# Kernel optimization log

Hardware: AMD Instinct MI355X
Metric: run time of the kernel (lower is better)

## Reference

```python
import jax, jax.numpy as jnp
import numpy as np

B_SZ, SEQ, IN_F, OUT_F, ST_F = 16, 4096, 256, 256, 256
RMIN, RMAX, MAX_PHASE = 0.9, 1.0, 6.283


def setup_inputs() -> dict:
    key = jax.random.key(0)
    ks = jax.random.split(key, 8)
    u1 = jax.random.uniform(ks[0], (ST_F,))
    u2 = jax.random.uniform(ks[1], (ST_F,))
    # same init math as the torch module
    nu_log = jnp.log(-0.5 * jnp.log(u1 * (RMAX + RMIN) * (RMAX - RMIN) + RMIN ** 2))
    theta_log = jnp.log(MAX_PHASE * u2)
    lam_abs = jnp.exp(-jnp.exp(nu_log))
    gamma_log = jnp.log(jnp.sqrt(1.0 - lam_abs ** 2))
    s2in = np.sqrt(2.0 * IN_F)
    B_re = jax.random.normal(ks[2], (ST_F, IN_F)) / s2in
    B_im = jax.random.normal(ks[3], (ST_F, IN_F)) / s2in
    sst = np.sqrt(ST_F)
    C_re = jax.random.normal(ks[4], (OUT_F, ST_F)) / sst
    C_im = jax.random.normal(ks[5], (OUT_F, ST_F)) / sst
    D = jax.random.normal(ks[6], (OUT_F, IN_F)) / np.sqrt(IN_F)
    inp = jax.random.normal(ks[7], (B_SZ, SEQ, IN_F), dtype=jnp.float32)
    return {"input": inp, "nu_log": nu_log, "theta_log": theta_log,
            "gamma_log": gamma_log, "B_re": B_re, "B_im": B_im,
            "C_re": C_re, "C_im": C_im, "D": D}


def _binop(a, b):
    # diagonal linear recurrence combine: (A, Bu)
    return (a[0] * b[0], b[0] * a[1] + b[1])


def reference(input, nu_log, theta_log, gamma_log, B_re, B_im, C_re, C_im, D):
    lam_abs = jnp.exp(-jnp.exp(nu_log))
    lam = (lam_abs * jnp.exp(1j * jnp.exp(theta_log))).astype(jnp.complex64)  # [N]
    gam = jnp.exp(gamma_log)[:, None]                                        # [N,1]
    Bm = (gam * (B_re + 1j * B_im)).astype(jnp.complex64)                    # [N,Hin]
    Cm = (C_re + 1j * C_im).astype(jnp.complex64)                            # [Hout,N]
    # Bu_t = B @ u_t  -> [B,L,N]
    Bu = jnp.einsum('blh,nh->bln', input.astype(jnp.complex64), Bm)
    lam_el = jnp.broadcast_to(lam, Bu.shape)
    # parallel associative scan over time: s_t = lam*s_{t-1} + Bu_t, s_{-1}=0
    _, s = jax.lax.associative_scan(_binop, (lam_el, Bu), axis=1)
    # module records the state BEFORE each update (initial state is zero)
    zero0 = jnp.zeros((input.shape[0], 1, lam.shape[0]), dtype=jnp.complex64)
    inner_states = jnp.concatenate([zero0, s[:, :-1, :]], axis=1)            # [B,L,N]
    output = jnp.einsum('bln,on->blo', inner_states, Cm).real \
             + jnp.einsum('blh,oh->blo', input, D)
    return output, inner_states
```

## Files before the change

kernel.cpp:

```cpp
#include <hip/hip_runtime.h>


typedef float  f32x4 __attribute__((ext_vector_type(4)));
typedef short  s16x8 __attribute__((ext_vector_type(8)));

__device__ __forceinline__ unsigned short f2bf(float x) {
  unsigned int u = __builtin_bit_cast(unsigned int, x);
  u += 0x7FFFu + ((u >> 16) & 1u);
  return (unsigned short)(u >> 16);
}
__device__ __forceinline__ float bf2f(unsigned int s) {
  unsigned int u = s << 16;
  return __builtin_bit_cast(float, u);
}
__device__ __forceinline__ f32x4 mfma16(s16x8 a, s16x8 b, f32x4 c) {
  return __builtin_amdgcn_mfma_f32_16x16x32_bf16(a, b, c, 0, 0, 0);
}

__global__ void k0_mix(const float* __restrict__ nu_log, const float* __restrict__ theta_log,
                       const float* __restrict__ gamma_log,
                       const float* __restrict__ B_re, const float* __restrict__ B_im,
                       const float* __restrict__ C_re, const float* __restrict__ C_im,
                       const float* __restrict__ Dm,
                       unsigned short* __restrict__ W1, float* __restrict__ W2f,
                       float* __restrict__ lamre, float* __restrict__ lamim,
                       float* __restrict__ lamLre, float* __restrict__ lamLim) {
  int idx = blockIdx.x * 256 + threadIdx.x;
  if (idx < 131072) {
    int ki = idx & 31; int np_ = (idx >> 5) & 511; int kk = idx >> 14;
    int k = kk * 32 + ki; int n = np_ & 255;
    float g = expf(gamma_log[n]);
    float v = (np_ < 256) ? B_re[n * 256 + k] : B_im[n * 256 + k];
    W1[idx] = f2bf(g * v);
  } else if (idx < 327680) {
    int j = idx - 131072;
    int k = j >> 8, o = j & 255;
    float v;
    if (k < 512) { int n = k >> 1; v = (k & 1) ? -C_im[o * 256 + n] : C_re[o * 256 + n]; }
    else         { v = Dm[o * 256 + (k - 512)]; }
    W2f[j] = v;
  } else if (idx < 327936) {
    int n = idx - 327680;
    float la = expf(-expf(nu_log[n]));
    float th = expf(theta_log[n]);
    float lr = la * cosf(th), li = la * sinf(th);
    lamre[n] = lr; lamim[n] = li;
    float r = lr, i = li;
    #pragma unroll
    for (int t = 0; t < 5; ++t) { float nr = r * r - i * i; float ni = 2.f * r * i; r = nr; i = ni; }
    lamLre[n] = r; lamLim[n] = i;
  }
}

__global__ void k0b_tile(const float* __restrict__ W2f, unsigned short* __restrict__ W2t) {
  int j = blockIdx.x * 256 + threadIdx.x;
  int ki = j & 31, o = (j >> 5) & 255, kk = j >> 13;
  W2t[j] = f2bf(W2f[(kk * 32 + ki) * 256 + o]);
}

__global__ __launch_bounds__(256, 3) void k1_red(const float* __restrict__ in,
                                                 const unsigned short* __restrict__ W1,
                                                 unsigned int* __restrict__ BuP,
                                                 const float* __restrict__ lamre,
                                                 const float* __restrict__ lamim,
                                                 float2* __restrict__ cl) {
  __shared__ unsigned short lA[64 * 264];
  __shared__ unsigned short lB[256 * 40];
  int tid = threadIdx.x;
  int bid = blockIdx.x;
  int nblk = bid & 1, mblk = bid >> 1;
  int M0 = mblk * 64, n0 = nblk * 128;
  int lane = tid & 63, wid = tid >> 6;
  int wm = wid >> 1, wn = wid & 1;

  #pragma unroll
  for (int pass = 0; pass < 16; ++pass) {
    int m = pass * 4 + (tid >> 6);
    int h0 = (tid & 63) * 4;
    float4 v = *reinterpret_cast<const float4*>(in + (size_t)(M0 + m) * 256 + h0);
    ushort4 s; s.x = f2bf(v.x); s.y = f2bf(v.y); s.z = f2bf(v.z); s.w = f2bf(v.w);
    *reinterpret_cast<ushort4*>(&lA[m * 264 + h0]) = s;
  }

  f32x4 acc[2][4][2];
  #pragma unroll
  for (int a = 0; a < 2; ++a)
    #pragma unroll
    for (int b = 0; b < 4; ++b)
      #pragma unroll
      for (int p = 0; p < 2; ++p) acc[a][b][p] = f32x4{0.f, 0.f, 0.f, 0.f};

  for (int kk = 0; kk < 8; ++kk) {
    __syncthreads();
    {
      const unsigned short* src_re = W1 + ((size_t)kk * 512 + n0) * 32;
      const unsigned short* src_im = W1 + ((size_t)kk * 512 + 256 + n0) * 32;
      #pragma unroll
      for (int half = 0; half < 2; ++half) {
        const unsigned short* src = half ? src_im : src_re;
        int rbase = half * 128;
        #pragma unroll
        for (int q = 0; q < 2; ++q) {
          int chunk = q * 256 + tid;
          int r = chunk >> 2, off = (chunk & 3) * 8;
          *reinterpret_cast<uint4*>(&lB[(rbase + r) * 40 + off]) =
              *reinterpret_cast<const uint4*>(src + r * 32 + off);
        }
      }
    }
    __syncthreads();
    s16x8 af[2];
    #pragma unroll
    for (int mt = 0; mt < 2; ++mt)
      af[mt] = *reinterpret_cast<const s16x8*>(
          &lA[(wm * 32 + mt * 16 + (lane & 15)) * 264 + kk * 32 + (lane >> 4) * 8]);
    #pragma unroll
    for (int nt = 0; nt < 4; ++nt) {
      #pragma unroll
      for (int p = 0; p < 2; ++p) {
        int r = p * 128 + wn * 64 + nt * 16 + (lane & 15);
        s16x8 bfr = *reinterpret_cast<const s16x8*>(&lB[r * 40 + (lane >> 4) * 8]);
        #pragma unroll
        for (int mt = 0; mt < 2; ++mt)
          acc[mt][nt][p] = mfma16(af[mt], bfr, acc[mt][nt][p]);
      }
    }
  }

  #pragma unroll
  for (int mt = 0; mt < 2; ++mt)
    #pragma unroll
    for (int nt = 0; nt < 4; ++nt)
      #pragma unroll
      for (int r = 0; r < 4; ++r) {
        int m = M0 + wm * 32 + mt * 16 + (lane >> 4) * 4 + r;
        int n = n0 + wn * 64 + nt * 16 + (lane & 15);
        unsigned int pk = (unsigned int)f2bf(acc[mt][nt][0][r]) |
                          ((unsigned int)f2bf(acc[mt][nt][1][r]) << 16);
        BuP[(size_t)m * 256 + n] = pk;
      }

  {
    int q = lane >> 4;
    #pragma unroll
    for (int nt = 0; nt < 4; ++nt) {
      int n = n0 + wn * 64 + nt * 16 + (lane & 15);
      float lr = lamre[n], li = lamim[n];
      float hr[2], hi[2];
      #pragma unroll
      for (int mt = 0; mt < 2; ++mt) {
        float xr = 0.f, xi = 0.f;
        #pragma unroll
        for (int r = 0; r < 4; ++r) {
          float br = acc[mt][nt][0][r], bi = acc[mt][nt][1][r];
          float nr2 = lr * xr - li * xi + br;
          float ni2 = lr * xi + li * xr + bi;
          xr = nr2; xi = ni2;
        }
        hr[mt] = xr; hi[mt] = xi;
      }
      float l2r = lr * lr - li * li, l2i = 2.f * lr * li;
      float l4r = l2r * l2r - l2i * l2i, l4i = 2.f * l2r * l2i;
      float p8r = l4r * l4r - l4i * l4i, p8i = 2.f * l4r * l4i;
      float p12r = p8r * l4r - p8i * l4i, p12i = p8r * l4i + p8i * l4r;
      float p16r = p8r * p8r - p8i * p8i, p16i = 2.f * p8r * p8i;
      float e1r, e1i;
      if (q == 0)      { e1r = p12r; e1i = p12i; }
      else if (q == 1) { e1r = p8r;  e1i = p8i;  }
      else if (q == 2) { e1r = l4r;  e1i = l4i;  }
      else             { e1r = 1.f;  e1i = 0.f;  }
      float e0r = e1r * p16r - e1i * p16i;
      float e0i = e1r * p16i + e1i * p16r;
      float Tr = e0r * hr[0] - e0i * hi[0] + e1r * hr[1] - e1i * hi[1];
      float Ti = e0r * hi[0] + e0i * hr[0] + e1r * hi[1] + e1i * hr[1];
      Tr += __shfl_xor(Tr, 16); Ti += __shfl_xor(Ti, 16);
      Tr += __shfl_xor(Tr, 32); Ti += __shfl_xor(Ti, 32);
      if (q == 0) {
        size_t C = (size_t)mblk * 2 + wm;
        cl[C * 256 + n] = make_float2(Tr, Ti);
      }
    }
  }
}

__global__ void k2b_scan(const float2* __restrict__ cl, float2* __restrict__ cin,
                         const float* __restrict__ lamLre, const float* __restrict__ lamLim) {
  int b = blockIdx.x, n = threadIdx.x;
  float lr = lamLre[n], li = lamLim[n];
  float sr = 0.f, si = 0.f;
  #pragma unroll 4
  for (int c = 0; c < 128; ++c) {
    size_t idx = ((size_t)b * 128 + c) * 256 + n;
    float2 L = cl[idx];
    cin[idx] = make_float2(sr, si);
    float nr = lr * sr - li * si + L.x;
    float ni = lr * si + li * sr + L.y;
    sr = nr; si = ni;
  }
}

__global__ __launch_bounds__(256) void k3a_scan(unsigned int* BuP, float* __restrict__ innerRe,
                                                const float2* __restrict__ cin,
                                                const float* __restrict__ lamre,
                                                const float* __restrict__ lamim) {
  int b = blockIdx.x >> 7, c = blockIdx.x & 127, n = threadIdx.x;
  size_t row0 = (size_t)b * 4096 + c * 32;
  float2 s0 = cin[((size_t)b * 128 + c) * 256 + n];
  float sr = s0.x, si = s0.y;
  float lr = lamre[n], li = lamim[n];
  #pragma unroll 4
  for (int j = 0; j < 32; ++j) {
    size_t idx = (row0 + j) * 256 + n;
    unsigned int v = BuP[idx];
    BuP[idx] = (unsigned int)f2bf(sr) | ((unsigned int)f2bf(si) << 16);
    innerRe[idx] = sr;
    float br = bf2f(v & 0xffffu), bi = bf2f(v >> 16);
    float nr = lr * sr - li * si + br;
    float ni = lr * si + li * sr + bi;
    sr = nr; si = ni;
  }
}

__global__ __launch_bounds__(1024, 4) void k3b_breg(const float* __restrict__ in,
                                                    const unsigned short* SPack,
                                                    const unsigned short* __restrict__ W2t,
                                                    float* outp) {
  __shared__ unsigned short lA[64 * 776];
  int tid = threadIdx.x, lane = tid & 63, w = tid >> 6;
  int l15 = lane & 15, q = lane >> 4;
  size_t row0 = (size_t)blockIdx.x * 64;

  s16x8 breg[2][4];
  auto loadB = [&](int buf, int p) {
    #pragma unroll
    for (int t = 0; t < 4; ++t) {
      int kk = p * 4 + t;
      int c = w * 16 + l15;
      breg[buf][t] = *reinterpret_cast<const s16x8*>(
          W2t + ((size_t)kk * 256 + c) * 32 + q * 8);
    }
  };

  loadB(0, 0);

  #pragma unroll
  for (int i = 0; i < 4; ++i) {
    int chunk = i * 1024 + tid;
    int r = chunk >> 6, c8 = (chunk & 63) * 8;
    *reinterpret_cast<uint4*>(&lA[r * 776 + c8]) =
        *reinterpret_cast<const uint4*>(SPack + (row0 + r) * 512 + c8);
  }
  #pragma unroll
  for (int i = 0; i < 4; ++i) {
    int chunk = i * 1024 + tid;
    int m = chunk >> 6, h0 = (chunk & 63) * 4;
    float4 v = *reinterpret_cast<const float4*>(in + (row0 + m) * 256 + h0);
    ushort4 s; s.x = f2bf(v.x); s.y = f2bf(v.y); s.z = f2bf(v.z); s.w = f2bf(v.w);
    *reinterpret_cast<ushort4*>(&lA[m * 776 + 512 + h0]) = s;
  }
  __syncthreads();

  f32x4 acc[4];
  #pragma unroll
  for (int mt = 0; mt < 4; ++mt) acc[mt] = f32x4{0.f, 0.f, 0.f, 0.f};

  #pragma unroll
  for (int p = 0; p < 6; ++p) {
    const int cur = p & 1;
    if (p < 5) loadB(cur ^ 1, p + 1);
    #pragma unroll
    for (int t = 0; t < 4; ++t) {
      int kk = p * 4 + t;
      #pragma unroll
      for (int mt = 0; mt < 4; ++mt) {
        s16x8 af = *reinterpret_cast<const s16x8*>(
            &lA[(mt * 16 + l15) * 776 + kk * 32 + q * 8]);
        acc[mt] = mfma16(af, breg[cur][t], acc[mt]);
      }
    }
  }

  #pragma unroll
  for (int mt = 0; mt < 4; ++mt)
    #pragma unroll
    for (int r = 0; r < 4; ++r) {
      size_t row = row0 + mt * 16 + q * 4 + r;
      int col = w * 16 + l15;
      outp[row * 256 + col] = acc[mt][r];
    }
}

extern "C" void kernel_launch(void* const* d_in, const int* in_sizes, int n_in,
                              void* d_out, int out_size, void* d_ws, size_t ws_size,
                              hipStream_t stream) {
  (void)in_sizes; (void)n_in; (void)out_size;
  const float* in       = (const float*)d_in[0];
  const float* nu_log   = (const float*)d_in[1];
  const float* theta_log= (const float*)d_in[2];
  const float* gamma_log= (const float*)d_in[3];
  const float* B_re     = (const float*)d_in[4];
  const float* B_im     = (const float*)d_in[5];
  const float* C_re     = (const float*)d_in[6];
  const float* C_im     = (const float*)d_in[7];
  const float* Dm       = (const float*)d_in[8];

  if (ws_size < (size_t)10 * 1024 * 1024) return;
  char* ws = (char*)d_ws;
  unsigned short* W1 = (unsigned short*)(ws + 0);
  float* W2f   = (float*)(ws + 262144);
  float* lamre  = (float*)(ws + 1048576);
  float* lamim  = lamre + 256;
  float* lamLre = lamre + 512;
  float* lamLim = lamre + 768;
  unsigned short* W2t = (unsigned short*)(ws + 1310720);
  float2* cl  = (float2*)(ws + (size_t)2 * 1024 * 1024);
  float2* cin = (float2*)(ws + (size_t)6 * 1024 * 1024);

  unsigned int* BuP = (unsigned int*)d_out;
  float* innerRe = (float*)d_out + (size_t)16777216;

  k0_mix<<<1281, 256, 0, stream>>>(nu_log, theta_log, gamma_log, B_re, B_im, C_re, C_im, Dm,
                                   W1, W2f, lamre, lamim, lamLre, lamLim);
  k0b_tile<<<768, 256, 0, stream>>>(W2f, W2t);
  k1_red<<<2048, 256, 0, stream>>>(in, W1, BuP, lamre, lamim, cl);
  k2b_scan<<<16, 256, 0, stream>>>(cl, cin, lamLre, lamLim);
  k3a_scan<<<2048, 256, 0, stream>>>(BuP, innerRe, cin, lamre, lamim);
  k3b_breg<<<1024, 1024, 0, stream>>>(in, (const unsigned short*)BuP, W2t, (float*)BuP);
}
```

Measured before the change: 166.1 us.

## Restructure Bu GEMM to 1024-thread blocks with register-resident double-buffered B fragments

The first GEMM kernel is rewritten so each 1024-thread block covers 64 rows across all 256 states, with each wave owning 16 state columns. The wave loads its B (weight) fragments directly from global memory into registers, double-buffered across k-phases, instead of staging them through shared memory with two barriers per k step. This halves the number of times each input tile is read and converted, and removes most block-level synchronization. In exchange it raises register pressure and makes the weight loads go straight to global memory or cache without LDS reuse. The chunk-summary reduction is adjusted to the new tile shape.

```diff
diff --git a/kernel.cpp b/kernel.cpp
--- a/kernel.cpp
+++ b/kernel.cpp
@@ -58,125 +58,111 @@
   W2t[j] = f2bf(W2f[(kk * 32 + ki) * 256 + o]);
 }
 
-__global__ __launch_bounds__(256, 3) void k1_red(const float* __restrict__ in,
-                                                 const unsigned short* __restrict__ W1,
-                                                 unsigned int* __restrict__ BuP,
-                                                 const float* __restrict__ lamre,
-                                                 const float* __restrict__ lamim,
-                                                 float2* __restrict__ cl) {
+__global__ __launch_bounds__(1024, 4) void k1_bstat(const float* __restrict__ in,
+                                                    const unsigned short* __restrict__ W1,
+                                                    unsigned int* __restrict__ BuP,
+                                                    const float* __restrict__ lamre,
+                                                    const float* __restrict__ lamim,
+                                                    float2* __restrict__ cl) {
   __shared__ unsigned short lA[64 * 264];
-  __shared__ unsigned short lB[256 * 40];
-  int tid = threadIdx.x;
-  int bid = blockIdx.x;
-  int nblk = bid & 1, mblk = bid >> 1;
-  int M0 = mblk * 64, n0 = nblk * 128;
-  int lane = tid & 63, wid = tid >> 6;
-  int wm = wid >> 1, wn = wid & 1;
-
-  #pragma unroll
-  for (int pass = 0; pass < 16; ++pass) {
-    int m = pass * 4 + (tid >> 6);
-    int h0 = (tid & 63) * 4;
-    float4 v = *reinterpret_cast<const float4*>(in + (size_t)(M0 + m) * 256 + h0);
+  int tid = threadIdx.x, lane = tid & 63, w = tid >> 6;
+  int l15 = lane & 15, q = lane >> 4;
+  int n = w * 16 + l15;
+  size_t row0 = (size_t)blockIdx.x * 64;
+
+  s16x8 breg[2][2][2];
+  auto loadB = [&](int buf, int ph) {
+    #pragma unroll
+    for (int p = 0; p < 2; ++p)
+      #pragma unroll
+      for (int t = 0; t < 2; ++t) {
+        int kk = ph * 2 + t;
+        breg[buf][p][t] = *reinterpret_cast<const s16x8*>(
+            W1 + (size_t)(kk * 512 + p * 256 + n) * 32 + q * 8);
+      }
+  };
+
+  loadB(0, 0);
+
+  #pragma unroll
+  for (int i = 0; i < 4; ++i) {
+    int chunk = i * 1024 + tid;
+    int m = chunk >> 6, h0 = (chunk & 63) * 4;
+    float4 v = *reinterpret_cast<const float4*>(in + (row0 + m) * 256 + h0);
     ushort4 s; s.x = f2bf(v.x); s.y = f2bf(v.y); s.z = f2bf(v.z); s.w = f2bf(v.w);
     *reinterpret_cast<ushort4*>(&lA[m * 264 + h0]) = s;
   }
-
-  f32x4 acc[2][4][2];
-  #pragma unroll
-  for (int a = 0; a < 2; ++a)
-    #pragma unroll
-    for (int b = 0; b < 4; ++b)
+  __syncthreads();
+
+  f32x4 acc[4][2];
+  #pragma unroll
+  for (int mt = 0; mt < 4; ++mt)
+    #pragma unroll
+    for (int p = 0; p < 2; ++p) acc[mt][p] = f32x4{0.f, 0.f, 0.f, 0.f};
+
+  #pragma unroll
+  for (int ph = 0; ph < 4; ++ph) {
+    const int cur = ph & 1;
+    if (ph < 3) loadB(cur ^ 1, ph + 1);
+    #pragma unroll
+    for (int t = 0; t < 2; ++t) {
+      int kk = ph * 2 + t;
       #pragma unroll
-      for (int p = 0; p < 2; ++p) acc[a][b][p] = f32x4{0.f, 0.f, 0.f, 0.f};
-
-  for (int kk = 0; kk < 8; ++kk) {
-    __syncthreads();
-    {
-      const unsigned short* src_re = W1 + ((size_t)kk * 512 + n0) * 32;
-      const unsigned short* src_im = W1 + ((size_t)kk * 512 + 256 + n0) * 32;
-      #pragma unroll
-      for (int half = 0; half < 2; ++half) {
-        const unsigned short* src = half ? src_im : src_re;
-        int rbase = half * 128;
-        #pragma unroll
-        for (int q = 0; q < 2; ++q) {
-          int chunk = q * 256 + tid;
-          int r = chunk >> 2, off = (chunk & 3) * 8;
-          *reinterpret_cast<uint4*>(&lB[(rbase + r) * 40 + off]) =
-              *reinterpret_cast<const uint4*>(src + r * 32 + off);
-        }
-      }
-    }
-    __syncthreads();
-    s16x8 af[2];
-    #pragma unroll
-    for (int mt = 0; mt < 2; ++mt)
-      af[mt] = *reinterpret_cast<const s16x8*>(
-          &lA[(wm * 32 + mt * 16 + (lane & 15)) * 264 + kk * 32 + (lane >> 4) * 8]);
-    #pragma unroll
-    for (int nt = 0; nt < 4; ++nt) {
-      #pragma unroll
-      for (int p = 0; p < 2; ++p) {
-        int r = p * 128 + wn * 64 + nt * 16 + (lane & 15);
-        s16x8 bfr = *reinterpret_cast<const s16x8*>(&lB[r * 40 + (lane >> 4) * 8]);
-        #pragma unroll
-        for (int mt = 0; mt < 2; ++mt)
-          acc[mt][nt][p] = mfma16(af[mt], bfr, acc[mt][nt][p]);
-      }
-    }
-  }
-
-  #pragma unroll
-  for (int mt = 0; mt < 2; ++mt)
-    #pragma unroll
-    for (int nt = 0; nt < 4; ++nt)
-      #pragma unroll
-      for (int r = 0; r < 4; ++r) {
-        int m = M0 + wm * 32 + mt * 16 + (lane >> 4) * 4 + r;
-        int n = n0 + wn * 64 + nt * 16 + (lane & 15);
-        unsigned int pk = (unsigned int)f2bf(acc[mt][nt][0][r]) |
-                          ((unsigned int)f2bf(acc[mt][nt][1][r]) << 16);
-        BuP[(size_t)m * 256 + n] = pk;
-      }
+      for (int mt = 0; mt < 4; ++mt) {
+        s16x8 af = *reinterpret_cast<const s16x8*>(
+            &lA[(mt * 16 + l15) * 264 + kk * 32 + q * 8]);
+        acc[mt][0] = mfma16(af, breg[cur][0][t], acc[mt][0]);
+        acc[mt][1] = mfma16(af, breg[cur][1][t], acc[mt][1]);
+      }
+    }
+  }
+
+  #pragma unroll
+  for (int mt = 0; mt < 4; ++mt)
+    #pragma unroll
+    for (int r = 0; r < 4; ++r) {
+      size_t row = row0 + mt * 16 + q * 4 + r;
+      unsigned int pk = (unsigned int)f2bf(acc[mt][0][r]) |
+                        ((unsigned int)f2bf(acc[mt][1][r]) << 16);
+      BuP[row * 256 + n] = pk;
+    }
 
   {
-    int q = lane >> 4;
-    #pragma unroll
-    for (int nt = 0; nt < 4; ++nt) {
-      int n = n0 + wn * 64 + nt * 16 + (lane & 15);
-      float lr = lamre[n], li = lamim[n];
+    float lr = lamre[n], li = lamim[n];
+    float l2r = lr * lr - li * li, l2i = 2.f * lr * li;
+    float l4r = l2r * l2r - l2i * l2i, l4i = 2.f * l2r * l2i;
+    float p8r = l4r * l4r - l4i * l4i, p8i = 2.f * l4r * l4i;
+    float p12r = p8r * l4r - p8i * l4i, p12i = p8r * l4i + p8i * l4r;
+    float p16r = p8r * p8r - p8i * p8i, p16i = 2.f * p8r * p8i;
+    float e1r, e1i;
+    if (q == 0)      { e1r = p12r; e1i = p12i; }
+    else if (q == 1) { e1r = p8r;  e1i = p8i;  }
+    else if (q == 2) { e1r = l4r;  e1i = l4i;  }
+    else             { e1r = 1.f;  e1i = 0.f;  }
+    float e0r = e1r * p16r - e1i * p16i;
+    float e0i = e1r * p16i + e1i * p16r;
+    #pragma unroll
+    for (int ch = 0; ch < 2; ++ch) {
       float hr[2], hi[2];
       #pragma unroll
-      for (int mt = 0; mt < 2; ++mt) {
+      for (int h = 0; h < 2; ++h) {
+        int mt = ch * 2 + h;
         float xr = 0.f, xi = 0.f;
         #pragma unroll
         for (int r = 0; r < 4; ++r) {
-          float br = acc[mt][nt][0][r], bi = acc[mt][nt][1][r];
+          float br = acc[mt][0][r], bi2 = acc[mt][1][r];
           float nr2 = lr * xr - li * xi + br;
-          float ni2 = lr * xi + li * xr + bi;
+          float ni2 = lr * xi + li * xr + bi2;
           xr = nr2; xi = ni2;
         }
-        hr[mt] = xr; hi[mt] = xi;
-      }
-      float l2r = lr * lr - li * li, l2i = 2.f * lr * li;
-      float l4r = l2r * l2r - l2i * l2i, l4i = 2.f * l2r * l2i;
-      float p8r = l4r * l4r - l4i * l4i, p8i = 2.f * l4r * l4i;
-      float p12r = p8r * l4r - p8i * l4i, p12i = p8r * l4i + p8i * l4r;
-      float p16r = p8r * p8r - p8i * p8i, p16i = 2.f * p8r * p8i;
-      float e1r, e1i;
-      if (q == 0)      { e1r = p12r; e1i = p12i; }
-      else if (q == 1) { e1r = p8r;  e1i = p8i;  }
-      else if (q == 2) { e1r = l4r;  e1i = l4i;  }
-      else             { e1r = 1.f;  e1i = 0.f;  }
-      float e0r = e1r * p16r - e1i * p16i;
-      float e0i = e1r * p16i + e1i * p16r;
+        hr[h] = xr; hi[h] = xi;
+      }
       float Tr = e0r * hr[0] - e0i * hi[0] + e1r * hr[1] - e1i * hi[1];
       float Ti = e0r * hi[0] + e0i * hr[0] + e1r * hi[1] + e1i * hr[1];
       Tr += __shfl_xor(Tr, 16); Ti += __shfl_xor(Ti, 16);
       Tr += __shfl_xor(Tr, 32); Ti += __shfl_xor(Ti, 32);
       if (q == 0) {
-        size_t C = (size_t)mblk * 2 + wm;
+        size_t C = (size_t)blockIdx.x * 2 + ch;
         cl[C * 256 + n] = make_float2(Tr, Ti);
       }
     }
@@ -322,7 +308,7 @@
   k0_mix<<<1281, 256, 0, stream>>>(nu_log, theta_log, gamma_log, B_re, B_im, C_re, C_im, Dm,
                                    W1, W2f, lamre, lamim, lamLre, lamLim);
   k0b_tile<<<768, 256, 0, stream>>>(W2f, W2t);
-  k1_red<<<2048, 256, 0, stream>>>(in, W1, BuP, lamre, lamim, cl);
+  k1_bstat<<<1024, 1024, 0, stream>>>(in, W1, BuP, lamre, lamim, cl);
   k2b_scan<<<16, 256, 0, stream>>>(cl, cin, lamLre, lamLim);
   k3a_scan<<<2048, 256, 0, stream>>>(BuP, innerRe, cin, lamre, lamim);
   k3b_breg<<<1024, 1024, 0, stream>>>(in, (const unsigned short*)BuP, W2t, (float*)BuP);
```

Result: faster. 146.1 us (-12.0%).
